# Optimization experiments

Measured on AMD Instinct MI355X. Metric: run time of the kernel, lower is better.

Reference implementation:

```python
import jax, jax.numpy as jnp
import numpy as np

N, C_IN, C_OUT = 8192, 256, 128
TEMP = 1.0
EDGE_P = 0.01  # Bernoulli edge probability -> avg degree ~82


def setup_inputs() -> dict:
    key = jax.random.key(0)
    k_x, k_adj, k_w, k_v0, k_v1 = jax.random.split(key, 5)
    node_feats = jax.random.normal(k_x, (N, C_IN), dtype=jnp.float32)
    adj_matrix = (jax.random.uniform(k_adj, (N, N)) < EDGE_P).astype(jnp.float32)
    lim_w = np.sqrt(6.0 / (C_IN + C_OUT))
    W = jax.random.uniform(k_w, (C_IN, C_OUT), minval=-lim_w, maxval=lim_w, dtype=jnp.float32)
    b = jnp.zeros((C_OUT,), dtype=jnp.float32)
    lim_v = np.sqrt(6.0 / (C_OUT + 1))
    v0 = jax.random.uniform(k_v0, (C_OUT,), minval=-lim_v, maxval=lim_v, dtype=jnp.float32)
    v1 = jax.random.uniform(k_v1, (C_OUT,), minval=-lim_v, maxval=lim_v, dtype=jnp.float32)
    return {"node_feats": node_feats, "adj_matrix": adj_matrix, "W": W, "b": b, "v0": v0, "v1": v1}


def reference(node_feats, adj_matrix, W, b, v0, v1):
    # h: [N, c_out]
    h = node_feats @ W + b
    f1 = h @ v0  # [N]
    f2 = h @ v1  # [N]
    # attn_logits = adj * (f1_i + f2_j); adj==0 entries become exact zeros,
    # which torch's .to_sparse() drops -> sparse softmax normalizes only
    # over edges (adj != 0), and empty rows densify to all-zero rows.
    logits = adj_matrix * (f1[:, None] + f2[None, :])
    vals = (jax.nn.sigmoid(logits) - 0.5) / TEMP
    mask = adj_matrix != 0
    masked = jnp.where(mask, vals, -jnp.inf)
    row_max = jnp.max(masked, axis=1, keepdims=True)
    row_max = jnp.where(jnp.isfinite(row_max), row_max, 0.0)  # guard empty rows
    e = jnp.where(mask, jnp.exp(masked - row_max), 0.0)
    denom = jnp.sum(e, axis=1, keepdims=True)
    attn_probs = e / jnp.maximum(denom, jnp.finfo(e.dtype).tiny)  # empty rows -> 0
    return attn_probs @ h
```

## Files before the change

kernel.cpp:

```cpp
#include <hip/hip_runtime.h>
#include <math.h>

#define NN    8192
#define CIN   256
#define COUT  128
#define NK1   512
#define MAXEG 256

typedef unsigned uvec4 __attribute__((ext_vector_type(4)));

__global__ __launch_bounds__(256) void kA(
    const float* __restrict__ X, const float* __restrict__ adj,
    const float* __restrict__ W, const float* __restrict__ b,
    const float* __restrict__ v0, const float* __restrict__ v1,
    float* __restrict__ h, float* __restrict__ f1, float* __restrict__ f2,
    unsigned* __restrict__ cnt, unsigned* __restrict__ outw)
{
    __shared__ float Xs[16][32];
    __shared__ unsigned scnt;
    __shared__ unsigned short sjl[MAXEG];

    const int tid = threadIdx.x;

    if (blockIdx.x < NK1) {
        const int ct  = tid & 63;
        const int rg  = tid >> 6;
        const int c   = ct * 2;
        const int row0 = blockIdx.x * 16;

        float acc[4][2] = {{0.f,0.f},{0.f,0.f},{0.f,0.f},{0.f,0.f}};

        for (int kc = 0; kc < CIN; kc += 32) {
            if (tid < 128) {
                const int r = tid >> 3, q = tid & 7;
                const float4 xv = *(const float4*)(X + (size_t)(row0 + r) * CIN + kc + q * 4);
                *(float4*)&Xs[r][q * 4] = xv;
            }
            float2 wv[32];
            #pragma unroll
            for (int kk = 0; kk < 32; ++kk)
                wv[kk] = *(const float2*)(W + (size_t)(kc + kk) * COUT + c);
            __syncthreads();

            #pragma unroll
            for (int rr = 0; rr < 4; ++rr) {
                const int lr = rg * 4 + rr;
                #pragma unroll
                for (int k4 = 0; k4 < 8; ++k4) {
                    const float4 xv = *(const float4*)&Xs[lr][k4 * 4];
                    acc[rr][0] += xv.x * wv[k4*4+0].x; acc[rr][1] += xv.x * wv[k4*4+0].y;
                    acc[rr][0] += xv.y * wv[k4*4+1].x; acc[rr][1] += xv.y * wv[k4*4+1].y;
                    acc[rr][0] += xv.z * wv[k4*4+2].x; acc[rr][1] += xv.z * wv[k4*4+2].y;
                    acc[rr][0] += xv.w * wv[k4*4+3].x; acc[rr][1] += xv.w * wv[k4*4+3].y;
                }
            }
            __syncthreads();
        }

        const float b0 = b[c], b1 = b[c+1];
        const float v00 = v0[c], v01 = v0[c+1];
        const float v10 = v1[c], v11 = v1[c+1];

        #pragma unroll
        for (int rr = 0; rr < 4; ++rr) {
            const int row = row0 + rg * 4 + rr;
            const float h0 = acc[rr][0] + b0;
            const float h1 = acc[rr][1] + b1;
            *(float2*)(h + (size_t)row * COUT + c) = make_float2(h0, h1);
            float p0 = h0 * v00 + h1 * v01;
            float p1 = h0 * v10 + h1 * v11;
            #pragma unroll
            for (int off = 32; off; off >>= 1) {
                p0 += __shfl_down(p0, off, 64);
                p1 += __shfl_down(p1, off, 64);
            }
            if (ct == 0) { f1[row] = p0; f2[row] = p1; }
        }
    } else {
        const int i = blockIdx.x - NK1;
        const uvec4* rowp = (const uvec4*)(adj + (size_t)i * NN);
        uvec4 v[8];
        #pragma unroll
        for (int it = 0; it < 8; ++it)
            v[it] = __builtin_nontemporal_load(rowp + tid + it * 256);

        if (tid == 0) scnt = 0;
        __syncthreads();

        #pragma unroll
        for (int it = 0; it < 8; ++it) {
            if (v[it].x | v[it].y | v[it].z | v[it].w) {
                const int j0 = (tid + it * 256) * 4;
                if (v[it].x) { const unsigned p = atomicAdd(&scnt, 1u); if (p < MAXEG) sjl[p] = (unsigned short)(j0    ); }
                if (v[it].y) { const unsigned p = atomicAdd(&scnt, 1u); if (p < MAXEG) sjl[p] = (unsigned short)(j0 + 1); }
                if (v[it].z) { const unsigned p = atomicAdd(&scnt, 1u); if (p < MAXEG) sjl[p] = (unsigned short)(j0 + 2); }
                if (v[it].w) { const unsigned p = atomicAdd(&scnt, 1u); if (p < MAXEG) sjl[p] = (unsigned short)(j0 + 3); }
            }
        }
        __syncthreads();

        if (tid < 128) {
            const unsigned w = (unsigned)sjl[2 * tid] | ((unsigned)sjl[2 * tid + 1] << 16);
            outw[(size_t)i * 128 + tid] = w;
        }
        if (tid == 0) cnt[i] = min(scnt, (unsigned)MAXEG);
    }
}

__global__ __launch_bounds__(256) void kB(
    const float* __restrict__ h, const float* __restrict__ f1,
    const float* __restrict__ f2, const unsigned* __restrict__ cnt,
    float* __restrict__ out)
{
    __shared__ unsigned short jl[MAXEG];
    __shared__ float  vl[MAXEG];
    __shared__ float  red[8];
    __shared__ float2 sacc[4][64];

    const int tid = threadIdx.x;
    const int i   = blockIdx.x;
    const int n   = (int)cnt[i];

    if (n == 0) {
        if (tid < COUT) out[(size_t)i * COUT + tid] = 0.f;
        return;
    }

    if (tid < 128) {
        const unsigned w = ((const unsigned*)out)[(size_t)i * 128 + tid];
        jl[2 * tid]     = (unsigned short)(w & 0xffffu);
        jl[2 * tid + 1] = (unsigned short)(w >> 16);
    }
    __syncthreads();

    float m = -1e30f;
    if (tid < n) {
        const float x = f1[i] + f2[jl[tid]];
        const float s = 1.f / (1.f + __expf(-x)) - 0.5f;
        vl[tid] = s;
        m = s;
    }
    #pragma unroll
    for (int off = 32; off; off >>= 1) m = fmaxf(m, __shfl_down(m, off, 64));
    if ((tid & 63) == 0) red[tid >> 6] = m;
    __syncthreads();
    m = fmaxf(fmaxf(red[0], red[1]), fmaxf(red[2], red[3]));

    float s = 0.f;
    if (tid < n) {
        s = __expf(vl[tid] - m);
        vl[tid] = s;
    }
    #pragma unroll
    for (int off = 32; off; off >>= 1) s += __shfl_down(s, off, 64);
    if ((tid & 63) == 0) red[4 + (tid >> 6)] = s;
    __syncthreads();
    const float inv = 1.f / (red[4] + red[5] + red[6] + red[7]);

    const int g  = tid >> 6;
    const int ct = tid & 63;
    const int c  = ct * 2;
    float ax = 0.f, ay = 0.f;
    int p = g;
    for (; p + 12 < n; p += 16) {
        const int   j0 = jl[p],     j1 = jl[p + 4], j2 = jl[p + 8], j3 = jl[p + 12];
        const float w0 = vl[p],     w1 = vl[p + 4], w2 = vl[p + 8], w3 = vl[p + 12];
        const float2 a0 = *(const float2*)(h + (size_t)j0 * COUT + c);
        const float2 a1 = *(const float2*)(h + (size_t)j1 * COUT + c);
        const float2 a2 = *(const float2*)(h + (size_t)j2 * COUT + c);
        const float2 a3 = *(const float2*)(h + (size_t)j3 * COUT + c);
        ax += w0 * a0.x + w1 * a1.x + w2 * a2.x + w3 * a3.x;
        ay += w0 * a0.y + w1 * a1.y + w2 * a2.y + w3 * a3.y;
    }
    for (; p < n; p += 4) {
        const int   j = jl[p];
        const float w = vl[p];
        const float2 a = *(const float2*)(h + (size_t)j * COUT + c);
        ax += w * a.x;
        ay += w * a.y;
    }
    sacc[g][ct] = make_float2(ax, ay);
    __syncthreads();
    if (tid < 64) {
        const float2 r0 = sacc[0][tid], r1 = sacc[1][tid];
        const float2 r2 = sacc[2][tid], r3 = sacc[3][tid];
        float2 r;
        r.x = (r0.x + r1.x + r2.x + r3.x) * inv;
        r.y = (r0.y + r1.y + r2.y + r3.y) * inv;
        *(float2*)(out + (size_t)i * COUT + tid * 2) = r;
    }
}

extern "C" void kernel_launch(void* const* d_in, const int* in_sizes, int n_in,
                              void* d_out, int out_size, void* d_ws, size_t ws_size,
                              hipStream_t stream) {
    const float* X   = (const float*)d_in[0];
    const float* adj = (const float*)d_in[1];
    const float* W   = (const float*)d_in[2];
    const float* b   = (const float*)d_in[3];
    const float* v0  = (const float*)d_in[4];
    const float* v1  = (const float*)d_in[5];
    float* out = (float*)d_out;

    float*    h   = (float*)d_ws;
    float*    f1  = h + (size_t)NN * COUT;
    float*    f2  = f1 + NN;
    unsigned* cnt = (unsigned*)(f2 + NN);

    kA<<<NK1 + NN, 256, 0, stream>>>(X, adj, W, b, v0, v1, h, f1, f2, cnt, (unsigned*)out);
    kB<<<NN, 256, 0, stream>>>(h, f1, f2, cnt, out);
}
```

Baseline: 88.41 us.

## Fuse adjacency scan with softmax-gather, multi-row blocks with double-buffered prefetch

Splits the GEMM into its own kernel. Fuses the adjacency row scan, the sparse softmax and the neighbor gather into one kernel in which each block handles 8 rows and prefetches the next row's adjacency into registers while the current row is processed. This removes the round trip of packed edge lists and counts through the output buffer and drops the second full-grid launch. It also replaces per-edge shared atomics with one atomic per nonzero vec4. In exchange, the adjacency scan no longer overlaps the GEMM, and holding two register buffers per thread with fewer blocks may reduce occupancy.

```diff
diff --git a/kernel.cpp b/kernel.cpp
--- a/kernel.cpp
+++ b/kernel.cpp
@@ -4,190 +4,201 @@
 #define NN    8192
 #define CIN   256
 #define COUT  128
-#define NK1   512
 #define MAXEG 256
+#define ROWS  8
+#define NBLK  (NN / ROWS)
 
 typedef unsigned uvec4 __attribute__((ext_vector_type(4)));
 
-__global__ __launch_bounds__(256) void kA(
-    const float* __restrict__ X, const float* __restrict__ adj,
-    const float* __restrict__ W, const float* __restrict__ b,
-    const float* __restrict__ v0, const float* __restrict__ v1,
-    float* __restrict__ h, float* __restrict__ f1, float* __restrict__ f2,
-    unsigned* __restrict__ cnt, unsigned* __restrict__ outw)
+__device__ __forceinline__ void bar_lds() {
+    asm volatile("s_waitcnt lgkmcnt(0)" ::: "memory");
+    __builtin_amdgcn_s_barrier();
+}
+
+__global__ __launch_bounds__(256) void k1_gemm(
+    const float* __restrict__ X, const float* __restrict__ W,
+    const float* __restrict__ b, const float* __restrict__ v0,
+    const float* __restrict__ v1,
+    float* __restrict__ h, float* __restrict__ f1, float* __restrict__ f2)
 {
     __shared__ float Xs[16][32];
+    const int tid = threadIdx.x;
+    const int ct  = tid & 63;
+    const int rg  = tid >> 6;
+    const int c   = ct * 2;
+    const int row0 = blockIdx.x * 16;
+
+    float acc[4][2] = {{0.f,0.f},{0.f,0.f},{0.f,0.f},{0.f,0.f}};
+
+    for (int kc = 0; kc < CIN; kc += 32) {
+        if (tid < 128) {
+            const int r = tid >> 3, q = tid & 7;
+            const float4 xv = *(const float4*)(X + (size_t)(row0 + r) * CIN + kc + q * 4);
+            *(float4*)&Xs[r][q * 4] = xv;
+        }
+        float2 wv[32];
+        #pragma unroll
+        for (int kk = 0; kk < 32; ++kk)
+            wv[kk] = *(const float2*)(W + (size_t)(kc + kk) * COUT + c);
+        __syncthreads();
+
+        #pragma unroll
+        for (int rr = 0; rr < 4; ++rr) {
+            const int lr = rg * 4 + rr;
+            #pragma unroll
+            for (int k4 = 0; k4 < 8; ++k4) {
+                const float4 xv = *(const float4*)&Xs[lr][k4 * 4];
+                acc[rr][0] += xv.x * wv[k4*4+0].x; acc[rr][1] += xv.x * wv[k4*4+0].y;
+                acc[rr][0] += xv.y * wv[k4*4+1].x; acc[rr][1] += xv.y * wv[k4*4+1].y;
+                acc[rr][0] += xv.z * wv[k4*4+2].x; acc[rr][1] += xv.z * wv[k4*4+2].y;
+                acc[rr][0] += xv.w * wv[k4*4+3].x; acc[rr][1] += xv.w * wv[k4*4+3].y;
+            }
+        }
+        __syncthreads();
+    }
+
+    const float b0 = b[c], b1 = b[c+1];
+    const float v00 = v0[c], v01 = v0[c+1];
+    const float v10 = v1[c], v11 = v1[c+1];
+
+    #pragma unroll
+    for (int rr = 0; rr < 4; ++rr) {
+        const int row = row0 + rg * 4 + rr;
+        const float h0 = acc[rr][0] + b0;
+        const float h1 = acc[rr][1] + b1;
+        *(float2*)(h + (size_t)row * COUT + c) = make_float2(h0, h1);
+        float p0 = h0 * v00 + h1 * v01;
+        float p1 = h0 * v10 + h1 * v11;
+        #pragma unroll
+        for (int off = 32; off; off >>= 1) {
+            p0 += __shfl_down(p0, off, 64);
+            p1 += __shfl_down(p1, off, 64);
+        }
+        if (ct == 0) { f1[row] = p0; f2[row] = p1; }
+    }
+}
+
+__device__ __forceinline__ void process_row(
+    const uvec4 (&cur)[8], const int row, const int tid,
+    const float* __restrict__ h, const float* __restrict__ f1,
+    const float* __restrict__ f2, float* __restrict__ out,
+    unsigned& scnt, unsigned short* sjl, float* vl, float* red,
+    float2 (*sacc)[64])
+{
+    if (tid == 0) scnt = 0;
+    bar_lds();
+
+    #pragma unroll
+    for (int it = 0; it < 8; ++it) {
+        const uvec4 v = cur[it];
+        if (v.x | v.y | v.z | v.w) {
+            const int j0 = (tid + it * 256) * 4;
+            const unsigned c4 = (v.x ? 1u : 0u) + (v.y ? 1u : 0u) +
+                                (v.z ? 1u : 0u) + (v.w ? 1u : 0u);
+            unsigned p = atomicAdd(&scnt, c4);
+            if (v.x) { if (p < MAXEG) sjl[p] = (unsigned short)(j0    ); ++p; }
+            if (v.y) { if (p < MAXEG) sjl[p] = (unsigned short)(j0 + 1); ++p; }
+            if (v.z) { if (p < MAXEG) sjl[p] = (unsigned short)(j0 + 2); ++p; }
+            if (v.w) { if (p < MAXEG) sjl[p] = (unsigned short)(j0 + 3); ++p; }
+        }
+    }
+    bar_lds();
+
+    const int n = min((int)scnt, (int)MAXEG);
+    if (n > 0) {
+        float m = -1e30f;
+        if (tid < n) {
+            const float x = f1[row] + f2[sjl[tid]];
+            const float s = 1.f / (1.f + __expf(-x)) - 0.5f;
+            vl[tid] = s;
+            m = s;
+        }
+        #pragma unroll
+        for (int off = 32; off; off >>= 1) m = fmaxf(m, __shfl_down(m, off, 64));
+        if ((tid & 63) == 0) red[tid >> 6] = m;
+        bar_lds();
+        m = fmaxf(fmaxf(red[0], red[1]), fmaxf(red[2], red[3]));
+
+        float s = 0.f;
+        if (tid < n) {
+            s = __expf(vl[tid] - m);
+            vl[tid] = s;
+        }
+        #pragma unroll
+        for (int off = 32; off; off >>= 1) s += __shfl_down(s, off, 64);
+        if ((tid & 63) == 0) red[4 + (tid >> 6)] = s;
+        bar_lds();
+        const float inv = 1.f / (red[4] + red[5] + red[6] + red[7]);
+
+        const int g  = tid >> 6;
+        const int ct = tid & 63;
+        const int c  = ct * 2;
+        float ax = 0.f, ay = 0.f;
+        int p = g;
+        for (; p + 12 < n; p += 16) {
+            const int   j0 = sjl[p],  j1 = sjl[p + 4], j2 = sjl[p + 8], j3 = sjl[p + 12];
+            const float w0 = vl[p],   w1 = vl[p + 4],  w2 = vl[p + 8],  w3 = vl[p + 12];
+            const float2 a0 = *(const float2*)(h + (size_t)j0 * COUT + c);
+            const float2 a1 = *(const float2*)(h + (size_t)j1 * COUT + c);
+            const float2 a2 = *(const float2*)(h + (size_t)j2 * COUT + c);
+            const float2 a3 = *(const float2*)(h + (size_t)j3 * COUT + c);
+            ax += w0 * a0.x + w1 * a1.x + w2 * a2.x + w3 * a3.x;
+            ay += w0 * a0.y + w1 * a1.y + w2 * a2.y + w3 * a3.y;
+        }
+        for (; p < n; p += 4) {
+            const int   j = sjl[p];
+            const float w = vl[p];
+            const float2 a = *(const float2*)(h + (size_t)j * COUT + c);
+            ax += w * a.x;
+            ay += w * a.y;
+        }
+        sacc[g][ct] = make_float2(ax, ay);
+        bar_lds();
+        if (tid < 64) {
+            const float2 r0 = sacc[0][tid], r1 = sacc[1][tid];
+            const float2 r2 = sacc[2][tid], r3 = sacc[3][tid];
+            float2 r;
+            r.x = (r0.x + r1.x + r2.x + r3.x) * inv;
+            r.y = (r0.y + r1.y + r2.y + r3.y) * inv;
+            *(float2*)(out + (size_t)row * COUT + tid * 2) = r;
+        }
+    } else {
+        if (tid < 64)
+            *(float2*)(out + (size_t)row * COUT + tid * 2) = make_float2(0.f, 0.f);
+    }
+}
+
+#define PREFETCH(BUF, PROW)                                                    \
+    {                                                                          \
+        const uvec4* rpn = (const uvec4*)(adj + (size_t)(PROW) * NN) + tid;    \
+        _Pragma("unroll")                                                      \
+        for (int it = 0; it < 8; ++it)                                         \
+            BUF[it] = __builtin_nontemporal_load(rpn + it * 256);              \
+    }
+
+__global__ __launch_bounds__(256) void k2_fused(
+    const float* __restrict__ adj, const float* __restrict__ h,
+    const float* __restrict__ f1, const float* __restrict__ f2,
+    float* __restrict__ out)
+{
     __shared__ unsigned scnt;
     __shared__ unsigned short sjl[MAXEG];
-
-    const int tid = threadIdx.x;
-
-    if (blockIdx.x < NK1) {
-        const int ct  = tid & 63;
-        const int rg  = tid >> 6;
-        const int c   = ct * 2;
-        const int row0 = blockIdx.x * 16;
-
-        float acc[4][2] = {{0.f,0.f},{0.f,0.f},{0.f,0.f},{0.f,0.f}};
-
-        for (int kc = 0; kc < CIN; kc += 32) {
-            if (tid < 128) {
-                const int r = tid >> 3, q = tid & 7;
-                const float4 xv = *(const float4*)(X + (size_t)(row0 + r) * CIN + kc + q * 4);
-                *(float4*)&Xs[r][q * 4] = xv;
-            }
-            float2 wv[32];
-            #pragma unroll
-            for (int kk = 0; kk < 32; ++kk)
-                wv[kk] = *(const float2*)(W + (size_t)(kc + kk) * COUT + c);
-            __syncthreads();
-
-            #pragma unroll
-            for (int rr = 0; rr < 4; ++rr) {
-                const int lr = rg * 4 + rr;
-                #pragma unroll
-                for (int k4 = 0; k4 < 8; ++k4) {
-                    const float4 xv = *(const float4*)&Xs[lr][k4 * 4];
-                    acc[rr][0] += xv.x * wv[k4*4+0].x; acc[rr][1] += xv.x * wv[k4*4+0].y;
-                    acc[rr][0] += xv.y * wv[k4*4+1].x; acc[rr][1] += xv.y * wv[k4*4+1].y;
-                    acc[rr][0] += xv.z * wv[k4*4+2].x; acc[rr][1] += xv.z * wv[k4*4+2].y;
-                    acc[rr][0] += xv.w * wv[k4*4+3].x; acc[rr][1] += xv.w * wv[k4*4+3].y;
-                }
-            }
-            __syncthreads();
-        }
-
-        const float b0 = b[c], b1 = b[c+1];
-        const float v00 = v0[c], v01 = v0[c+1];
-        const float v10 = v1[c], v11 = v1[c+1];
-
-        #pragma unroll
-        for (int rr = 0; rr < 4; ++rr) {
-            const int row = row0 + rg * 4 + rr;
-            const float h0 = acc[rr][0] + b0;
-            const float h1 = acc[rr][1] + b1;
-            *(float2*)(h + (size_t)row * COUT + c) = make_float2(h0, h1);
-            float p0 = h0 * v00 + h1 * v01;
-            float p1 = h0 * v10 + h1 * v11;
-            #pragma unroll
-            for (int off = 32; off; off >>= 1) {
-                p0 += __shfl_down(p0, off, 64);
-                p1 += __shfl_down(p1, off, 64);
-            }
-            if (ct == 0) { f1[row] = p0; f2[row] = p1; }
-        }
-    } else {
-        const int i = blockIdx.x - NK1;
-        const uvec4* rowp = (const uvec4*)(adj + (size_t)i * NN);
-        uvec4 v[8];
-        #pragma unroll
-        for (int it = 0; it < 8; ++it)
-            v[it] = __builtin_nontemporal_load(rowp + tid + it * 256);
-
-        if (tid == 0) scnt = 0;
-        __syncthreads();
-
-        #pragma unroll
-        for (int it = 0; it < 8; ++it) {
-            if (v[it].x | v[it].y | v[it].z | v[it].w) {
-                const int j0 = (tid + it * 256) * 4;
-                if (v[it].x) { const unsigned p = atomicAdd(&scnt, 1u); if (p < MAXEG) sjl[p] = (unsigned short)(j0    ); }
-                if (v[it].y) { const unsigned p = atomicAdd(&scnt, 1u); if (p < MAXEG) sjl[p] = (unsigned short)(j0 + 1); }
-                if (v[it].z) { const unsigned p = atomicAdd(&scnt, 1u); if (p < MAXEG) sjl[p] = (unsigned short)(j0 + 2); }
-                if (v[it].w) { const unsigned p = atomicAdd(&scnt, 1u); if (p < MAXEG) sjl[p] = (unsigned short)(j0 + 3); }
-            }
-        }
-        __syncthreads();
-
-        if (tid < 128) {
-            const unsigned w = (unsigned)sjl[2 * tid] | ((unsigned)sjl[2 * tid + 1] << 16);
-            outw[(size_t)i * 128 + tid] = w;
-        }
-        if (tid == 0) cnt[i] = min(scnt, (unsigned)MAXEG);
-    }
-}
-
-__global__ __launch_bounds__(256) void kB(
-    const float* __restrict__ h, const float* __restrict__ f1,
-    const float* __restrict__ f2, const unsigned* __restrict__ cnt,
-    float* __restrict__ out)
-{
-    __shared__ unsigned short jl[MAXEG];
     __shared__ float  vl[MAXEG];
     __shared__ float  red[8];
     __shared__ float2 sacc[4][64];
 
-    const int tid = threadIdx.x;
-    const int i   = blockIdx.x;
-    const int n   = (int)cnt[i];
-
-    if (n == 0) {
-        if (tid < COUT) out[(size_t)i * COUT + tid] = 0.f;
-        return;
-    }
-
-    if (tid < 128) {
-        const unsigned w = ((const unsigned*)out)[(size_t)i * 128 + tid];
-        jl[2 * tid]     = (unsigned short)(w & 0xffffu);
-        jl[2 * tid + 1] = (unsigned short)(w >> 16);
-    }
-    __syncthreads();
-
-    float m = -1e30f;
-    if (tid < n) {
-        const float x = f1[i] + f2[jl[tid]];
-        const float s = 1.f / (1.f + __expf(-x)) - 0.5f;
-        vl[tid] = s;
-        m = s;
-    }
-    #pragma unroll
-    for (int off = 32; off; off >>= 1) m = fmaxf(m, __shfl_down(m, off, 64));
-    if ((tid & 63) == 0) red[tid >> 6] = m;
-    __syncthreads();
-    m = fmaxf(fmaxf(red[0], red[1]), fmaxf(red[2], red[3]));
-
-    float s = 0.f;
-    if (tid < n) {
-        s = __expf(vl[tid] - m);
-        vl[tid] = s;
-    }
-    #pragma unroll
-    for (int off = 32; off; off >>= 1) s += __shfl_down(s, off, 64);
-    if ((tid & 63) == 0) red[4 + (tid >> 6)] = s;
-    __syncthreads();
-    const float inv = 1.f / (red[4] + red[5] + red[6] + red[7]);
-
-    const int g  = tid >> 6;
-    const int ct = tid & 63;
-    const int c  = ct * 2;
-    float ax = 0.f, ay = 0.f;
-    int p = g;
-    for (; p + 12 < n; p += 16) {
-        const int   j0 = jl[p],     j1 = jl[p + 4], j2 = jl[p + 8], j3 = jl[p + 12];
-        const float w0 = vl[p],     w1 = vl[p + 4], w2 = vl[p + 8], w3 = vl[p + 12];
-        const float2 a0 = *(const float2*)(h + (size_t)j0 * COUT + c);
-        const float2 a1 = *(const float2*)(h + (size_t)j1 * COUT + c);
-        const float2 a2 = *(const float2*)(h + (size_t)j2 * COUT + c);
-        const float2 a3 = *(const float2*)(h + (size_t)j3 * COUT + c);
-        ax += w0 * a0.x + w1 * a1.x + w2 * a2.x + w3 * a3.x;
-        ay += w0 * a0.y + w1 * a1.y + w2 * a2.y + w3 * a3.y;
-    }
-    for (; p < n; p += 4) {
-        const int   j = jl[p];
-        const float w = vl[p];
-        const float2 a = *(const float2*)(h + (size_t)j * COUT + c);
-        ax += w * a.x;
-        ay += w * a.y;
-    }
-    sacc[g][ct] = make_float2(ax, ay);
-    __syncthreads();
-    if (tid < 64) {
-        const float2 r0 = sacc[0][tid], r1 = sacc[1][tid];
-        const float2 r2 = sacc[2][tid], r3 = sacc[3][tid];
-        float2 r;
-        r.x = (r0.x + r1.x + r2.x + r3.x) * inv;
-        r.y = (r0.y + r1.y + r2.y + r3.y) * inv;
-        *(float2*)(out + (size_t)i * COUT + tid * 2) = r;
+    const int tid  = threadIdx.x;
+    const int row0 = blockIdx.x * ROWS;
+
+    uvec4 va[8], vb[8];
+    PREFETCH(va, row0)
+
+    #pragma unroll 1
+    for (int rp = 0; rp < ROWS; rp += 2) {
+        PREFETCH(vb, row0 + rp + 1)
+        process_row(va, row0 + rp, tid, h, f1, f2, out, scnt, sjl, vl, red, sacc);
+        if (rp + 2 < ROWS) PREFETCH(va, row0 + rp + 2)
+        process_row(vb, row0 + rp + 1, tid, h, f1, f2, out, scnt, sjl, vl, red, sacc);
     }
 }
 
@@ -202,11 +213,10 @@
     const float* v1  = (const float*)d_in[5];
     float* out = (float*)d_out;
 
-    float*    h   = (float*)d_ws;
-    float*    f1  = h + (size_t)NN * COUT;
-    float*    f2  = f1 + NN;
-    unsigned* cnt = (unsigned*)(f2 + NN);
-
-    kA<<<NK1 + NN, 256, 0, stream>>>(X, adj, W, b, v0, v1, h, f1, f2, cnt, (unsigned*)out);
-    kB<<<NN, 256, 0, stream>>>(h, f1, f2, cnt, out);
-}
+    float* h  = (float*)d_ws;
+    float* f1 = h + (size_t)NN * COUT;
+    float* f2 = f1 + NN;
+
+    k1_gemm<<<NN / 16, 256, 0, stream>>>(X, W, b, v0, v1, h, f1, f2);
+    k2_fused<<<NBLK, 256, 0, stream>>>(adj, h, f1, f2, out);
+}
```

Result: slower. 143.1 us (+61.9%).

## Split GEMM and adjacency scan into separate kernels, use one wavefront per row

Applied to the files above, without the earlier changes.

The combined GEMM-plus-scan kernel becomes two kernels: a GEMM kernel and an adjacency scan kernel. The scan kernel gives each wavefront one row and builds the edge list with a ballot-style bitmask plus a wave prefix scan, replacing shared-memory atomics. The aggregation kernel now processes one row per wavefront, with no block-wide syncs or cross-wave reduction. This adds a kernel launch and loses overlap between the GEMM and the scan. Edge order is now deterministic, and each wave walks its whole neighbour list serially, which lengthens per-row latency.

```diff
diff --git a/kernel.cpp b/kernel.cpp
--- a/kernel.cpp
+++ b/kernel.cpp
@@ -4,107 +4,128 @@
 #define NN    8192
 #define CIN   256
 #define COUT  128
-#define NK1   512
 #define MAXEG 256
 
 typedef unsigned uvec4 __attribute__((ext_vector_type(4)));
 
-__global__ __launch_bounds__(256) void kA(
-    const float* __restrict__ X, const float* __restrict__ adj,
-    const float* __restrict__ W, const float* __restrict__ b,
-    const float* __restrict__ v0, const float* __restrict__ v1,
-    float* __restrict__ h, float* __restrict__ f1, float* __restrict__ f2,
-    unsigned* __restrict__ cnt, unsigned* __restrict__ outw)
+__global__ __launch_bounds__(256) void k1_gemm(
+    const float* __restrict__ X, const float* __restrict__ W,
+    const float* __restrict__ b, const float* __restrict__ v0,
+    const float* __restrict__ v1,
+    float* __restrict__ h, float* __restrict__ f1, float* __restrict__ f2)
 {
     __shared__ float Xs[16][32];
-    __shared__ unsigned scnt;
-    __shared__ unsigned short sjl[MAXEG];
-
     const int tid = threadIdx.x;
-
-    if (blockIdx.x < NK1) {
-        const int ct  = tid & 63;
-        const int rg  = tid >> 6;
-        const int c   = ct * 2;
-        const int row0 = blockIdx.x * 16;
-
-        float acc[4][2] = {{0.f,0.f},{0.f,0.f},{0.f,0.f},{0.f,0.f}};
-
-        for (int kc = 0; kc < CIN; kc += 32) {
-            if (tid < 128) {
-                const int r = tid >> 3, q = tid & 7;
-                const float4 xv = *(const float4*)(X + (size_t)(row0 + r) * CIN + kc + q * 4);
-                *(float4*)&Xs[r][q * 4] = xv;
+    const int ct  = tid & 63;
+    const int rg  = tid >> 6;
+    const int c   = ct * 2;
+    const int row0 = blockIdx.x * 16;
+
+    float acc[4][2] = {{0.f,0.f},{0.f,0.f},{0.f,0.f},{0.f,0.f}};
+
+    for (int kc = 0; kc < CIN; kc += 32) {
+        if (tid < 128) {
+            const int r = tid >> 3, q = tid & 7;
+            const float4 xv = *(const float4*)(X + (size_t)(row0 + r) * CIN + kc + q * 4);
+            *(float4*)&Xs[r][q * 4] = xv;
+        }
+        float2 wv[32];
+        #pragma unroll
+        for (int kk = 0; kk < 32; ++kk)
+            wv[kk] = *(const float2*)(W + (size_t)(kc + kk) * COUT + c);
+        __syncthreads();
+
+        #pragma unroll
+        for (int rr = 0; rr < 4; ++rr) {
+            const int lr = rg * 4 + rr;
+            #pragma unroll
+            for (int k4 = 0; k4 < 8; ++k4) {
+                const float4 xv = *(const float4*)&Xs[lr][k4 * 4];
+                acc[rr][0] += xv.x * wv[k4*4+0].x; acc[rr][1] += xv.x * wv[k4*4+0].y;
+                acc[rr][0] += xv.y * wv[k4*4+1].x; acc[rr][1] += xv.y * wv[k4*4+1].y;
+                acc[rr][0] += xv.z * wv[k4*4+2].x; acc[rr][1] += xv.z * wv[k4*4+2].y;
+                acc[rr][0] += xv.w * wv[k4*4+3].x; acc[rr][1] += xv.w * wv[k4*4+3].y;
             }
-            float2 wv[32];
-            #pragma unroll
-            for (int kk = 0; kk < 32; ++kk)
-                wv[kk] = *(const float2*)(W + (size_t)(kc + kk) * COUT + c);
-            __syncthreads();
-
-            #pragma unroll
-            for (int rr = 0; rr < 4; ++rr) {
-                const int lr = rg * 4 + rr;
-                #pragma unroll
-                for (int k4 = 0; k4 < 8; ++k4) {
-                    const float4 xv = *(const float4*)&Xs[lr][k4 * 4];
-                    acc[rr][0] += xv.x * wv[k4*4+0].x; acc[rr][1] += xv.x * wv[k4*4+0].y;
-                    acc[rr][0] += xv.y * wv[k4*4+1].x; acc[rr][1] += xv.y * wv[k4*4+1].y;
-                    acc[rr][0] += xv.z * wv[k4*4+2].x; acc[rr][1] += xv.z * wv[k4*4+2].y;
-                    acc[rr][0] += xv.w * wv[k4*4+3].x; acc[rr][1] += xv.w * wv[k4*4+3].y;
-                }
-            }
-            __syncthreads();
-        }
-
-        const float b0 = b[c], b1 = b[c+1];
-        const float v00 = v0[c], v01 = v0[c+1];
-        const float v10 = v1[c], v11 = v1[c+1];
-
-        #pragma unroll
-        for (int rr = 0; rr < 4; ++rr) {
-            const int row = row0 + rg * 4 + rr;
-            const float h0 = acc[rr][0] + b0;
-            const float h1 = acc[rr][1] + b1;
-            *(float2*)(h + (size_t)row * COUT + c) = make_float2(h0, h1);
-            float p0 = h0 * v00 + h1 * v01;
-            float p1 = h0 * v10 + h1 * v11;
-            #pragma unroll
-            for (int off = 32; off; off >>= 1) {
-                p0 += __shfl_down(p0, off, 64);
-                p1 += __shfl_down(p1, off, 64);
-            }
-            if (ct == 0) { f1[row] = p0; f2[row] = p1; }
-        }
-    } else {
-        const int i = blockIdx.x - NK1;
-        const uvec4* rowp = (const uvec4*)(adj + (size_t)i * NN);
+        }
+        __syncthreads();
+    }
+
+    const float b0 = b[c], b1 = b[c+1];
+    const float v00 = v0[c], v01 = v0[c+1];
+    const float v10 = v1[c], v11 = v1[c+1];
+
+    #pragma unroll
+    for (int rr = 0; rr < 4; ++rr) {
+        const int row = row0 + rg * 4 + rr;
+        const float h0 = acc[rr][0] + b0;
+        const float h1 = acc[rr][1] + b1;
+        *(float2*)(h + (size_t)row * COUT + c) = make_float2(h0, h1);
+        float p0 = h0 * v00 + h1 * v01;
+        float p1 = h0 * v10 + h1 * v11;
+        #pragma unroll
+        for (int off = 32; off; off >>= 1) {
+            p0 += __shfl_down(p0, off, 64);
+            p1 += __shfl_down(p1, off, 64);
+        }
+        if (ct == 0) { f1[row] = p0; f2[row] = p1; }
+    }
+}
+
+__global__ __launch_bounds__(256) void k_scan(
+    const float* __restrict__ adj, unsigned* __restrict__ cnt,
+    unsigned* __restrict__ outw)
+{
+    __shared__ unsigned short sjl[4][MAXEG];
+    const int tid  = threadIdx.x;
+    const int wid  = tid >> 6;
+    const int lane = tid & 63;
+    const int row  = blockIdx.x * 4 + wid;
+    const uvec4* rowp = (const uvec4*)(adj + (size_t)row * NN);
+    unsigned wcnt = 0;
+
+    #pragma unroll
+    for (int b = 0; b < 4; ++b) {
         uvec4 v[8];
         #pragma unroll
         for (int it = 0; it < 8; ++it)
-            v[it] = __builtin_nontemporal_load(rowp + tid + it * 256);
-
-        if (tid == 0) scnt = 0;
-        __syncthreads();
-
+            v[it] = __builtin_nontemporal_load(rowp + b * 512 + it * 64 + lane);
+
+        unsigned lm = 0;
         #pragma unroll
         for (int it = 0; it < 8; ++it) {
-            if (v[it].x | v[it].y | v[it].z | v[it].w) {
-                const int j0 = (tid + it * 256) * 4;
-                if (v[it].x) { const unsigned p = atomicAdd(&scnt, 1u); if (p < MAXEG) sjl[p] = (unsigned short)(j0    ); }
-                if (v[it].y) { const unsigned p = atomicAdd(&scnt, 1u); if (p < MAXEG) sjl[p] = (unsigned short)(j0 + 1); }
-                if (v[it].z) { const unsigned p = atomicAdd(&scnt, 1u); if (p < MAXEG) sjl[p] = (unsigned short)(j0 + 2); }
-                if (v[it].w) { const unsigned p = atomicAdd(&scnt, 1u); if (p < MAXEG) sjl[p] = (unsigned short)(j0 + 3); }
-            }
-        }
-        __syncthreads();
-
-        if (tid < 128) {
-            const unsigned w = (unsigned)sjl[2 * tid] | ((unsigned)sjl[2 * tid + 1] << 16);
-            outw[(size_t)i * 128 + tid] = w;
-        }
-        if (tid == 0) cnt[i] = min(scnt, (unsigned)MAXEG);
-    }
+            const unsigned m4 = ((v[it].x >> 23) & 1u) | ((v[it].y >> 22) & 2u) |
+                                ((v[it].z >> 21) & 4u) | ((v[it].w >> 20) & 8u);
+            lm |= m4 << (it * 4);
+        }
+
+        const int lc = __popc(lm);
+        int pre = lc;
+        #pragma unroll
+        for (int off = 1; off < 64; off <<= 1) {
+            const int t = __shfl_up(pre, off, 64);
+            if (lane >= off) pre += t;
+        }
+        unsigned basep = wcnt + (unsigned)(pre - lc);
+        wcnt += (unsigned)__shfl(pre, 63, 64);
+
+        unsigned mm = lm;
+        while (mm) {
+            const int bit = __builtin_ctz(mm);
+            mm &= mm - 1;
+            const unsigned j = (unsigned)((b * 512 + (bit >> 2) * 64 + lane) * 4 + (bit & 3));
+            if (basep < MAXEG) sjl[wid][basep] = (unsigned short)j;
+            ++basep;
+        }
+    }
+
+    asm volatile("s_waitcnt lgkmcnt(0)" ::: "memory");
+    #pragma unroll
+    for (int r = 0; r < 2; ++r) {
+        const int k = lane + r * 64;
+        const unsigned w = (unsigned)sjl[wid][2 * k] | ((unsigned)sjl[wid][2 * k + 1] << 16);
+        outw[(size_t)row * 128 + k] = w;
+    }
+    if (lane == 0) cnt[row] = min(wcnt, (unsigned)MAXEG);
 }
 
 __global__ __launch_bounds__(256) void kB(
@@ -112,59 +133,66 @@
     const float* __restrict__ f2, const unsigned* __restrict__ cnt,
     float* __restrict__ out)
 {
-    __shared__ unsigned short jl[MAXEG];
-    __shared__ float  vl[MAXEG];
-    __shared__ float  red[8];
-    __shared__ float2 sacc[4][64];
-
-    const int tid = threadIdx.x;
-    const int i   = blockIdx.x;
-    const int n   = (int)cnt[i];
+    __shared__ unsigned short jl[4][MAXEG];
+    __shared__ float vl[4][MAXEG];
+    const int tid  = threadIdx.x;
+    const int wid  = tid >> 6;
+    const int lane = tid & 63;
+    const int i    = blockIdx.x * 4 + wid;
+    const int n    = (int)cnt[i];
+    const int c    = lane * 2;
 
     if (n == 0) {
-        if (tid < COUT) out[(size_t)i * COUT + tid] = 0.f;
+        *(float2*)(out + (size_t)i * COUT + c) = make_float2(0.f, 0.f);
         return;
     }
 
-    if (tid < 128) {
-        const unsigned w = ((const unsigned*)out)[(size_t)i * 128 + tid];
-        jl[2 * tid]     = (unsigned short)(w & 0xffffu);
-        jl[2 * tid + 1] = (unsigned short)(w >> 16);
-    }
-    __syncthreads();
-
+    #pragma unroll
+    for (int r = 0; r < 2; ++r) {
+        const int k = lane + r * 64;
+        const unsigned w = ((const unsigned*)out)[(size_t)i * 128 + k];
+        jl[wid][2 * k]     = (unsigned short)(w & 0xffffu);
+        jl[wid][2 * k + 1] = (unsigned short)(w >> 16);
+    }
+    asm volatile("s_waitcnt lgkmcnt(0)" ::: "memory");
+
+    const float f1i = f1[i];
     float m = -1e30f;
-    if (tid < n) {
-        const float x = f1[i] + f2[jl[tid]];
-        const float s = 1.f / (1.f + __expf(-x)) - 0.5f;
-        vl[tid] = s;
-        m = s;
-    }
-    #pragma unroll
-    for (int off = 32; off; off >>= 1) m = fmaxf(m, __shfl_down(m, off, 64));
-    if ((tid & 63) == 0) red[tid >> 6] = m;
-    __syncthreads();
-    m = fmaxf(fmaxf(red[0], red[1]), fmaxf(red[2], red[3]));
-
-    float s = 0.f;
-    if (tid < n) {
-        s = __expf(vl[tid] - m);
-        vl[tid] = s;
-    }
-    #pragma unroll
-    for (int off = 32; off; off >>= 1) s += __shfl_down(s, off, 64);
-    if ((tid & 63) == 0) red[4 + (tid >> 6)] = s;
-    __syncthreads();
-    const float inv = 1.f / (red[4] + red[5] + red[6] + red[7]);
-
-    const int g  = tid >> 6;
-    const int ct = tid & 63;
-    const int c  = ct * 2;
+    #pragma unroll
+    for (int q = 0; q < 4; ++q) {
+        const int p = lane + q * 64;
+        if (p < n) {
+            const float x = f1i + f2[jl[wid][p]];
+            const float s = 1.f / (1.f + __expf(-x)) - 0.5f;
+            vl[wid][p] = s;
+            m = fmaxf(m, s);
+        }
+    }
+    #pragma unroll
+    for (int off = 32; off; off >>= 1) m = fmaxf(m, __shfl_xor(m, off, 64));
+
+    float ssum = 0.f;
+    #pragma unroll
+    for (int q = 0; q < 4; ++q) {
+        const int p = lane + q * 64;
+        if (p < n) {
+            const float e = __expf(vl[wid][p] - m);
+            vl[wid][p] = e;
+            ssum += e;
+        }
+    }
+    #pragma unroll
+    for (int off = 32; off; off >>= 1) ssum += __shfl_xor(ssum, off, 64);
+    const float inv = 1.f / ssum;
+    asm volatile("s_waitcnt lgkmcnt(0)" ::: "memory");
+
     float ax = 0.f, ay = 0.f;
-    int p = g;
-    for (; p + 12 < n; p += 16) {
-        const int   j0 = jl[p],     j1 = jl[p + 4], j2 = jl[p + 8], j3 = jl[p + 12];
-        const float w0 = vl[p],     w1 = vl[p + 4], w2 = vl[p + 8], w3 = vl[p + 12];
+    int p = 0;
+    for (; p + 3 < n; p += 4) {
+        const int   j0 = jl[wid][p],     j1 = jl[wid][p + 1];
+        const int   j2 = jl[wid][p + 2], j3 = jl[wid][p + 3];
+        const float w0 = vl[wid][p],     w1 = vl[wid][p + 1];
+        const float w2 = vl[wid][p + 2], w3 = vl[wid][p + 3];
         const float2 a0 = *(const float2*)(h + (size_t)j0 * COUT + c);
         const float2 a1 = *(const float2*)(h + (size_t)j1 * COUT + c);
         const float2 a2 = *(const float2*)(h + (size_t)j2 * COUT + c);
@@ -172,23 +200,14 @@
         ax += w0 * a0.x + w1 * a1.x + w2 * a2.x + w3 * a3.x;
         ay += w0 * a0.y + w1 * a1.y + w2 * a2.y + w3 * a3.y;
     }
-    for (; p < n; p += 4) {
-        const int   j = jl[p];
-        const float w = vl[p];
+    for (; p < n; ++p) {
+        const int   j = jl[wid][p];
+        const float w = vl[wid][p];
         const float2 a = *(const float2*)(h + (size_t)j * COUT + c);
         ax += w * a.x;
         ay += w * a.y;
     }
-    sacc[g][ct] = make_float2(ax, ay);
-    __syncthreads();
-    if (tid < 64) {
-        const float2 r0 = sacc[0][tid], r1 = sacc[1][tid];
-        const float2 r2 = sacc[2][tid], r3 = sacc[3][tid];
-        float2 r;
-        r.x = (r0.x + r1.x + r2.x + r3.x) * inv;
-        r.y = (r0.y + r1.y + r2.y + r3.y) * inv;
-        *(float2*)(out + (size_t)i * COUT + tid * 2) = r;
-    }
+    *(float2*)(out + (size_t)i * COUT + c) = make_float2(ax * inv, ay * inv);
 }
 
 extern "C" void kernel_launch(void* const* d_in, const int* in_sizes, int n_in,
@@ -207,6 +226,7 @@
     float*    f2  = f1 + NN;
     unsigned* cnt = (unsigned*)(f2 + NN);
 
-    kA<<<NK1 + NN, 256, 0, stream>>>(X, adj, W, b, v0, v1, h, f1, f2, cnt, (unsigned*)out);
-    kB<<<NN, 256, 0, stream>>>(h, f1, f2, cnt, out);
-}
+    k1_gemm<<<NN / 16, 256, 0, stream>>>(X, W, b, v0, v1, h, f1, f2);
+    k_scan<<<NN / 4, 256, 0, stream>>>(adj, cnt, (unsigned*)out);
+    kB<<<NN / 4, 256, 0, stream>>>(h, f1, f2, cnt, out);
+}
```

Result: slower. 99.79 us (+12.9%).
